# Kernel tuning notes

Hardware: AMD Instinct MI355X
Metric: run time of the kernel (lower is better)

Reference implementation:

```python
import jax, jax.numpy as jnp
import numpy as np

N = 40000
IN_DIM = 128
HID = 64
E = 640000


def sage_conv(x, edge_index, W_l, b_l, W_r):
    """PyG SAGEConv with mean aggregation.
    out = lin_l(mean_{j in N(i)} x_j) + lin_r(x_i)
    edge_index[0]=src (message source), edge_index[1]=dst (aggregation target).
    """
    src, dst = edge_index[0], edge_index[1]
    n = x.shape[0]
    msgs = x[src]                                            # [E, d] gather
    sums = jax.ops.segment_sum(msgs, dst, num_segments=n)    # [N, d]
    cnt = jax.ops.segment_sum(jnp.ones((msgs.shape[0],), x.dtype), dst,
                              num_segments=n)                # [N]
    mean = sums / jnp.maximum(cnt, 1.0)[:, None]
    return mean @ W_l.T + b_l + x @ W_r.T


def setup_inputs() -> dict:
    key = jax.random.key(0)
    ks = jax.random.split(key, 8)
    x = jax.random.normal(ks[0], (N, IN_DIM), dtype=jnp.float32)
    edge_index = jax.random.randint(ks[1], (2, E), 0, N, dtype=jnp.int32)
    s1 = 1.0 / np.sqrt(IN_DIM)
    s2 = 1.0 / np.sqrt(HID)
    W1_l = jax.random.uniform(ks[2], (HID, IN_DIM), jnp.float32, -s1, s1)
    b1_l = jax.random.uniform(ks[3], (HID,), jnp.float32, -s1, s1)
    W1_r = jax.random.uniform(ks[4], (HID, IN_DIM), jnp.float32, -s1, s1)
    W2_l = jax.random.uniform(ks[5], (HID, HID), jnp.float32, -s2, s2)
    b2_l = jax.random.uniform(ks[6], (HID,), jnp.float32, -s2, s2)
    W2_r = jax.random.uniform(ks[7], (HID, HID), jnp.float32, -s2, s2)
    return {"x": x, "edge_index": edge_index,
            "W1_l": W1_l, "b1_l": b1_l, "W1_r": W1_r,
            "W2_l": W2_l, "b2_l": b2_l, "W2_r": W2_r}


def reference(x, edge_index, W1_l, b1_l, W1_r, W2_l, b2_l, W2_r):
    h = sage_conv(x, edge_index, W1_l, b1_l, W1_r)
    h = jax.nn.relu(h)
    # dropout is identity in eval mode (reference baseline is deterministic)
    z = sage_conv(h, edge_index, W2_l, b2_l, W2_r)
    return z
```

## Files before the change

### kernel.cpp

```cpp
#include <hip/hip_runtime.h>

#define INDIM 128
#define HID 64
#define CAP 64
#define GEMM_BLOCKS 625
#define BIN_BLOCKS 256
#define PREP_BLOCKS 32
#define RSH 7
#define RMASK ((1 << RSH) - 1)
#define NRANGE 313
#define SBCAP 28

__device__ __forceinline__ float bf2f(unsigned short u) {
    union { unsigned int i; float f; } c; c.i = ((unsigned int)u) << 16; return c.f;
}
__device__ __forceinline__ unsigned short f2bf(float f) {
    union { float f; unsigned int i; } c; c.f = f;
    return (unsigned short)((c.i + 0x7FFFu + ((c.i >> 16) & 1u)) >> 16);
}

__device__ __forceinline__ void agg8(const unsigned short* __restrict__ Pb,
                                     int idx0, int deg, int q, int f8,
                                     float acc[8]) {
    const int nstep = (deg + 7) >> 3;
    for (int s = 0; s < nstep; s += 2) {
        #pragma unroll
        for (int u = 0; u < 2; ++u) {
            const int ss = s + u;
            const int lanesel = ss * 8 + q;
            const int sidx = __shfl(idx0, lanesel, 64);
            const float m = (ss < nstep && lanesel < deg) ? 1.f : 0.f;
            const uint4 v = *(const uint4*)&Pb[(size_t)sidx * 64 + f8 * 8];
            acc[0] += bf2f((unsigned short)(v.x & 0xffffu)) * m;
            acc[1] += bf2f((unsigned short)(v.x >> 16)) * m;
            acc[2] += bf2f((unsigned short)(v.y & 0xffffu)) * m;
            acc[3] += bf2f((unsigned short)(v.y >> 16)) * m;
            acc[4] += bf2f((unsigned short)(v.z & 0xffffu)) * m;
            acc[5] += bf2f((unsigned short)(v.z >> 16)) * m;
            acc[6] += bf2f((unsigned short)(v.w & 0xffffu)) * m;
            acc[7] += bf2f((unsigned short)(v.w >> 16)) * m;
        }
    }
    #pragma unroll
    for (int j = 0; j < 8; ++j) {
        acc[j] += __shfl_xor(acc[j], 8, 64);
        acc[j] += __shfl_xor(acc[j], 16, 64);
        acc[j] += __shfl_xor(acc[j], 32, 64);
    }
}


__global__ __launch_bounds__(256) void k_bin_prep(
    const int* __restrict__ src, const int* __restrict__ dst,
    unsigned int* __restrict__ hist_global, unsigned int* __restrict__ ebin,
    const float* __restrict__ W1l, const float* __restrict__ W1r,
    const float* __restrict__ W2l, const float* __restrict__ W2r,
    float* __restrict__ WT1l, float* __restrict__ WT1r,
    float* __restrict__ WT2l, float* __restrict__ WT2r, int E) {
    const int tid = threadIdx.x;

    if (blockIdx.x >= BIN_BLOCKS) {
        const int gtid = (blockIdx.x - BIN_BLOCKS) * 256 + tid;
        if (gtid < 64 * 128) {
            int j = gtid >> 7, k = gtid & 127;
            WT1l[k * 64 + j] = W1l[gtid];
            WT1r[k * 64 + j] = W1r[gtid];
        }
        if (gtid < 64 * 64) {
            int j = gtid >> 6, k = gtid & 63;
            WT2l[k * 64 + j] = W2l[gtid];
            WT2r[k * 64 + j] = W2r[gtid];
        }
        return;
    }

    __shared__ unsigned int hist[NRANGE];
    __shared__ unsigned int cur[NRANGE];
    const int b = blockIdx.x;
    const int ech = (E + BIN_BLOCKS - 1) / BIN_BLOCKS;
    const int e0 = b * ech;
    const int e1 = (e0 + ech < E) ? e0 + ech : E;

    for (int r = tid; r < NRANGE; r += 256) { hist[r] = 0; cur[r] = 0; }
    __syncthreads();
    for (int e = e0 + tid; e < e1; e += 256)
        atomicAdd(&hist[((unsigned)dst[e]) >> RSH], 1u);
    __syncthreads();
    for (int r = tid; r < NRANGE; r += 256)
        hist_global[(size_t)r * BIN_BLOCKS + b] = hist[r];
    __syncthreads();
    for (int e = e0 + tid; e < e1; e += 256) {
        const unsigned d = (unsigned)dst[e];
        const unsigned s = (unsigned)src[e];
        const unsigned r = d >> RSH;
        const unsigned off = atomicAdd(&cur[r], 1u);
        if (off < SBCAP)
            ebin[((size_t)r * BIN_BLOCKS + b) * SBCAP + off] = (d << 16) | s;
    }
}


__global__ __launch_bounds__(256) void k_gemm1_place(
    const float* __restrict__ A,
    const float* __restrict__ WTl, const float* __restrict__ WTr,
    unsigned short* __restrict__ Pb, float* __restrict__ Q,
    const unsigned int* __restrict__ hist_global,
    const unsigned int* __restrict__ ebin,
    int* __restrict__ cnt, unsigned short* __restrict__ sorted, int N) {
    __shared__ float As[64][INDIM + 1];
    __shared__ unsigned int lcnt[1 << RSH];
    const int tid = threadIdx.x;

    if (blockIdx.x < NRANGE) {
        const int r = blockIdx.x;
        if (tid < (1 << RSH)) lcnt[tid] = 0;
        __syncthreads();
        unsigned c = hist_global[(size_t)r * BIN_BLOCKS + tid];
        if (c > SBCAP) c = SBCAP;
        const unsigned int* eb = ebin + ((size_t)r * BIN_BLOCKS + tid) * SBCAP;
        for (unsigned i = 0; i < c; ++i) {
            const unsigned p = eb[i];
            const unsigned d = p >> 16;
            const unsigned slot = atomicAdd(&lcnt[d & RMASK], 1u);
            if (slot < CAP)
                sorted[(d << 6) + slot] = (unsigned short)(p & 0xffffu);
        }
        __syncthreads();
        for (int l = tid; l < (1 << RSH); l += 256) {
            const int node = (r << RSH) + l;
            if (node < N) cnt[node] = (int)lcnt[l];
        }
        return;
    }

    const int bm = (blockIdx.x - NRANGE) * 64;
    for (int idx = tid; idx < 64 * 32; idx += 256) {
        int row = idx >> 5, kq = idx & 31;
        const float4 v = ((const float4*)A)[(size_t)(bm + row) * 32 + kq];
        As[row][kq * 4 + 0] = v.x; As[row][kq * 4 + 1] = v.y;
        As[row][kq * 4 + 2] = v.z; As[row][kq * 4 + 3] = v.w;
    }
    __syncthreads();

    const int tx = tid & 15, ty = tid >> 4;
    const int n0 = ty * 4;
    float accl[4][4] = {}, accr[4][4] = {};
    #pragma unroll 8
    for (int k = 0; k < INDIM; ++k) {
        float a[4];
        #pragma unroll
        for (int i = 0; i < 4; ++i) a[i] = As[n0 + i][k];
        const float4 blv = ((const float4*)WTl)[k * 16 + tx];
        const float4 brv = ((const float4*)WTr)[k * 16 + tx];
        const float bl[4] = {blv.x, blv.y, blv.z, blv.w};
        const float br[4] = {brv.x, brv.y, brv.z, brv.w};
        #pragma unroll
        for (int i = 0; i < 4; ++i) {
            #pragma unroll
            for (int j = 0; j < 4; ++j) {
                accl[i][j] += a[i] * bl[j];
                accr[i][j] += a[i] * br[j];
            }
        }
    }
    #pragma unroll
    for (int i = 0; i < 4; ++i) {
        int m = bm + n0 + i;
        ushort4 pv;
        pv.x = f2bf(accl[i][0]); pv.y = f2bf(accl[i][1]);
        pv.z = f2bf(accl[i][2]); pv.w = f2bf(accl[i][3]);
        ((ushort4*)Pb)[(size_t)m * 16 + tx] = pv;
        ((float4*)Q)[(size_t)m * 16 + tx] =
            make_float4(accr[i][0], accr[i][1], accr[i][2], accr[i][3]);
    }
}


__global__ __launch_bounds__(256) void k_agg1(
    const unsigned short* __restrict__ Pb, const float* __restrict__ Q,
    const float* __restrict__ b1,
    const int* __restrict__ cnt, const unsigned short* __restrict__ sorted,
    unsigned short* __restrict__ Hb, float* __restrict__ H, int N) {
    const int wid  = (blockIdx.x * 256 + threadIdx.x) >> 6;
    const int lane = threadIdx.x & 63;
    const int q = lane >> 3, f8 = lane & 7;
    if (wid >= N) return;
    int deg = cnt[wid]; if (deg > CAP) deg = CAP;
    const int ls = (lane < deg) ? lane : ((deg > 0) ? deg - 1 : 0);
    const int idx0 = (deg > 0) ? (int)sorted[(wid << 6) + ls] : 0;
    float acc[8] = {};
    agg8(Pb, idx0, deg, q, f8, acc);
    if (q == 0) {
        const float inv = 1.0f / fmaxf((float)deg, 1.0f);
        const float4 qa = *(const float4*)&Q[(size_t)wid * 64 + f8 * 8];
        const float4 qb = *(const float4*)&Q[(size_t)wid * 64 + f8 * 8 + 4];
        const float4 ba = *(const float4*)&b1[f8 * 8];
        const float4 bb = *(const float4*)&b1[f8 * 8 + 4];
        float h0 = fmaxf(acc[0] * inv + ba.x + qa.x, 0.f);
        float h1 = fmaxf(acc[1] * inv + ba.y + qa.y, 0.f);
        float h2 = fmaxf(acc[2] * inv + ba.z + qa.z, 0.f);
        float h3 = fmaxf(acc[3] * inv + ba.w + qa.w, 0.f);
        float h4 = fmaxf(acc[4] * inv + bb.x + qb.x, 0.f);
        float h5 = fmaxf(acc[5] * inv + bb.y + qb.y, 0.f);
        float h6 = fmaxf(acc[6] * inv + bb.z + qb.z, 0.f);
        float h7 = fmaxf(acc[7] * inv + bb.w + qb.w, 0.f);
        uint4 u;
        u.x = (unsigned)f2bf(h0) | ((unsigned)f2bf(h1) << 16);
        u.y = (unsigned)f2bf(h2) | ((unsigned)f2bf(h3) << 16);
        u.z = (unsigned)f2bf(h4) | ((unsigned)f2bf(h5) << 16);
        u.w = (unsigned)f2bf(h6) | ((unsigned)f2bf(h7) << 16);
        *(uint4*)&Hb[(size_t)wid * 64 + f8 * 8] = u;
        *(float4*)&H[(size_t)wid * 64 + f8 * 8] = make_float4(h0, h1, h2, h3);
        *(float4*)&H[(size_t)wid * 64 + f8 * 8 + 4] = make_float4(h4, h5, h6, h7);
    }
}


__global__ __launch_bounds__(256) void k_agg2h(
    const unsigned short* __restrict__ Hb,
    const int* __restrict__ cnt, const unsigned short* __restrict__ sorted,
    float* __restrict__ meanH, int N) {
    const int wid  = (blockIdx.x * 256 + threadIdx.x) >> 6;
    const int lane = threadIdx.x & 63;
    const int q = lane >> 3, f8 = lane & 7;
    if (wid >= N) return;
    int deg = cnt[wid]; if (deg > CAP) deg = CAP;
    const int ls = (lane < deg) ? lane : ((deg > 0) ? deg - 1 : 0);
    const int idx0 = (deg > 0) ? (int)sorted[(wid << 6) + ls] : 0;
    float acc[8] = {};
    agg8(Hb, idx0, deg, q, f8, acc);
    if (q == 0) {
        const float inv = 1.0f / fmaxf((float)deg, 1.0f);
        *(float4*)&meanH[(size_t)wid * 64 + f8 * 8] =
            make_float4(acc[0] * inv, acc[1] * inv, acc[2] * inv, acc[3] * inv);
        *(float4*)&meanH[(size_t)wid * 64 + f8 * 8 + 4] =
            make_float4(acc[4] * inv, acc[5] * inv, acc[6] * inv, acc[7] * inv);
    }
}


__global__ __launch_bounds__(256) void k_gemm_z(
    const float* __restrict__ meanH, const float* __restrict__ H,
    const float* __restrict__ WTl, const float* __restrict__ WTr,
    const float* __restrict__ b2, float* __restrict__ z, int N) {
    __shared__ float As1[64][HID + 1];
    __shared__ float As2[64][HID + 1];
    const int tid = threadIdx.x;
    const int bm = blockIdx.x * 64;
    for (int idx = tid; idx < 64 * 16; idx += 256) {
        int row = idx >> 4, kq = idx & 15;
        const float4 v1 = ((const float4*)meanH)[(size_t)(bm + row) * 16 + kq];
        const float4 v2 = ((const float4*)H)[(size_t)(bm + row) * 16 + kq];
        As1[row][kq * 4 + 0] = v1.x; As1[row][kq * 4 + 1] = v1.y;
        As1[row][kq * 4 + 2] = v1.z; As1[row][kq * 4 + 3] = v1.w;
        As2[row][kq * 4 + 0] = v2.x; As2[row][kq * 4 + 1] = v2.y;
        As2[row][kq * 4 + 2] = v2.z; As2[row][kq * 4 + 3] = v2.w;
    }
    __syncthreads();

    const int tx = tid & 15, ty = tid >> 4;
    const int n0 = ty * 4;
    float acc[4][4] = {};
    #pragma unroll 8
    for (int k = 0; k < HID; ++k) {
        float a1[4], a2[4];
        #pragma unroll
        for (int i = 0; i < 4; ++i) { a1[i] = As1[n0 + i][k]; a2[i] = As2[n0 + i][k]; }
        const float4 blv = ((const float4*)WTl)[k * 16 + tx];
        const float4 brv = ((const float4*)WTr)[k * 16 + tx];
        const float bl[4] = {blv.x, blv.y, blv.z, blv.w};
        const float br[4] = {brv.x, brv.y, brv.z, brv.w};
        #pragma unroll
        for (int i = 0; i < 4; ++i) {
            #pragma unroll
            for (int j = 0; j < 4; ++j)
                acc[i][j] += a1[i] * bl[j] + a2[i] * br[j];
        }
    }
    const float4 bv = *(const float4*)&b2[tx * 4];
    #pragma unroll
    for (int i = 0; i < 4; ++i) {
        int m = bm + n0 + i;
        if (m < N) {
            ((float4*)z)[(size_t)m * 16 + tx] =
                make_float4(acc[i][0] + bv.x, acc[i][1] + bv.y,
                            acc[i][2] + bv.z, acc[i][3] + bv.w);
        }
    }
}


extern "C" void kernel_launch(void* const* d_in, const int* in_sizes, int n_in,
                              void* d_out, int out_size, void* d_ws, size_t ws_size,
                              hipStream_t stream) {
    const float* x   = (const float*)d_in[0];
    const int*  edge = (const int*)d_in[1];
    const float* W1l = (const float*)d_in[2];
    const float* b1l = (const float*)d_in[3];
    const float* W1r = (const float*)d_in[4];
    const float* W2l = (const float*)d_in[5];
    const float* b2l = (const float*)d_in[6];
    const float* W2r = (const float*)d_in[7];

    const int N = in_sizes[0] / INDIM;
    const int E = in_sizes[1] / 2;
    const int* src = edge;
    const int* dst = edge + E;

    char* w = (char*)d_ws;
    auto carve = [&](size_t bytes) {
        char* p = w; w += (bytes + 255) & ~(size_t)255; return p;
    };
    unsigned short* Pb  = (unsigned short*)carve((size_t)N * 64 * 2);
    unsigned short* Hb  = (unsigned short*)carve((size_t)N * 64 * 2);
    float* Q     = (float*)carve((size_t)N * 64 * 4);
    float* H     = (float*)carve((size_t)N * 64 * 4);
    float* meanH = (float*)carve((size_t)N * 64 * 4);
    float* WT1l = (float*)carve(128 * 64 * 4);
    float* WT1r = (float*)carve(128 * 64 * 4);
    float* WT2l = (float*)carve(64 * 64 * 4);
    float* WT2r = (float*)carve(64 * 64 * 4);
    int* cnt    = (int*)carve((size_t)N * 4);
    unsigned short* sorted = (unsigned short*)carve((size_t)N * CAP * 2);
    unsigned int* hist_global = (unsigned int*)carve((size_t)NRANGE * BIN_BLOCKS * 4);
    unsigned int* ebin = (unsigned int*)carve((size_t)NRANGE * BIN_BLOCKS * SBCAP * 4);

    float* zout = (float*)d_out;

    const int gT = (N + 63) / 64;
    const int gW = (N * 64 + 255) / 256;

    k_bin_prep<<<BIN_BLOCKS + PREP_BLOCKS, 256, 0, stream>>>(
        src, dst, hist_global, ebin,
        W1l, W1r, W2l, W2r, WT1l, WT1r, WT2l, WT2r, E);
    k_gemm1_place<<<NRANGE + GEMM_BLOCKS, 256, 0, stream>>>(
        x, WT1l, WT1r, Pb, Q, hist_global, ebin, cnt, sorted, N);
    k_agg1<<<gW, 256, 0, stream>>>(Pb, Q, b1l, cnt, sorted, Hb, H, N);
    k_agg2h<<<gW, 256, 0, stream>>>(Hb, cnt, sorted, meanH, N);
    k_gemm_z<<<gT, 256, 0, stream>>>(meanH, H, WT2l, WT2r, b2l, zout, N);
}
```

Measured before the change: 109.9 us.

## Aggregate with 32 lanes per edge row and parallelize bin placement across lanes

Measured after the change: 108.8 us. About the same (-0.9%).

```diff
diff --git a/kernel.cpp b/kernel.cpp
--- a/kernel.cpp
+++ b/kernel.cpp
@@ -11,42 +11,32 @@
 #define NRANGE 313
 #define SBCAP 28
 
-__device__ __forceinline__ float bf2f(unsigned short u) {
-    union { unsigned int i; float f; } c; c.i = ((unsigned int)u) << 16; return c.f;
-}
 __device__ __forceinline__ unsigned short f2bf(float f) {
     union { float f; unsigned int i; } c; c.f = f;
     return (unsigned short)((c.i + 0x7FFFu + ((c.i >> 16) & 1u)) >> 16);
 }
 
-__device__ __forceinline__ void agg8(const unsigned short* __restrict__ Pb,
-                                     int idx0, int deg, int q, int f8,
-                                     float acc[8]) {
-    const int nstep = (deg + 7) >> 3;
-    for (int s = 0; s < nstep; s += 2) {
-        #pragma unroll
-        for (int u = 0; u < 2; ++u) {
-            const int ss = s + u;
-            const int lanesel = ss * 8 + q;
-            const int sidx = __shfl(idx0, lanesel, 64);
-            const float m = (ss < nstep && lanesel < deg) ? 1.f : 0.f;
-            const uint4 v = *(const uint4*)&Pb[(size_t)sidx * 64 + f8 * 8];
-            acc[0] += bf2f((unsigned short)(v.x & 0xffffu)) * m;
-            acc[1] += bf2f((unsigned short)(v.x >> 16)) * m;
-            acc[2] += bf2f((unsigned short)(v.y & 0xffffu)) * m;
-            acc[3] += bf2f((unsigned short)(v.y >> 16)) * m;
-            acc[4] += bf2f((unsigned short)(v.z & 0xffffu)) * m;
-            acc[5] += bf2f((unsigned short)(v.z >> 16)) * m;
-            acc[6] += bf2f((unsigned short)(v.w & 0xffffu)) * m;
-            acc[7] += bf2f((unsigned short)(v.w >> 16)) * m;
-        }
-    }
-    #pragma unroll
-    for (int j = 0; j < 8; ++j) {
-        acc[j] += __shfl_xor(acc[j], 8, 64);
-        acc[j] += __shfl_xor(acc[j], 16, 64);
-        acc[j] += __shfl_xor(acc[j], 32, 64);
-    }
+__device__ __forceinline__ void aggF(const unsigned short* __restrict__ T,
+                                     int idxv, int deg, int f2,
+                                     float& a0, float& a1) {
+    const int eo = (threadIdx.x & 63) >> 5;
+    for (int s = 0; s < deg; s += 8) {
+        #pragma unroll
+        for (int u = 0; u < 4; ++u) {
+            const int e = s + u * 2 + eo;
+            int sidx = __shfl(idxv, e, 64);
+            const bool live = (e < deg);
+            sidx = live ? sidx : 0;
+            const unsigned uu = *(const unsigned*)&T[(size_t)sidx * 64 + f2 * 2];
+            union { unsigned i; float f; } clo, chi;
+            clo.i = uu << 16;
+            chi.i = uu & 0xffff0000u;
+            a0 += live ? clo.f : 0.f;
+            a1 += live ? chi.f : 0.f;
+        }
+    }
+    a0 += __shfl_xor(a0, 32, 64);
+    a1 += __shfl_xor(a1, 32, 64);
 }
 
 
@@ -115,15 +105,23 @@
         const int r = blockIdx.x;
         if (tid < (1 << RSH)) lcnt[tid] = 0;
         __syncthreads();
-        unsigned c = hist_global[(size_t)r * BIN_BLOCKS + tid];
-        if (c > SBCAP) c = SBCAP;
-        const unsigned int* eb = ebin + ((size_t)r * BIN_BLOCKS + tid) * SBCAP;
-        for (unsigned i = 0; i < c; ++i) {
-            const unsigned p = eb[i];
-            const unsigned d = p >> 16;
-            const unsigned slot = atomicAdd(&lcnt[d & RMASK], 1u);
-            if (slot < CAP)
-                sorted[(d << 6) + slot] = (unsigned short)(p & 0xffffu);
+        const int lane = tid & 63, w = tid >> 6;
+        const int sb_local = lane >> 3, ent0 = lane & 7;
+        for (int g = w * 8; g < BIN_BLOCKS; g += 32) {
+            const int sb = g + sb_local;
+            unsigned c = hist_global[(size_t)r * BIN_BLOCKS + sb];
+            if (c > SBCAP) c = SBCAP;
+            const unsigned int* eb = ebin + ((size_t)r * BIN_BLOCKS + sb) * SBCAP;
+            for (unsigned p = 0; p * 8 < c; ++p) {
+                const unsigned e = p * 8 + ent0;
+                if (e < c) {
+                    const unsigned pkt = eb[e];
+                    const unsigned d = pkt >> 16;
+                    const unsigned slot = atomicAdd(&lcnt[d & RMASK], 1u);
+                    if (slot < CAP)
+                        sorted[(d << 6) + slot] = (unsigned short)(pkt & 0xffffu);
+                }
+            }
         }
         __syncthreads();
         for (int l = tid; l < (1 << RSH); l += 256) {
@@ -183,35 +181,21 @@
     unsigned short* __restrict__ Hb, float* __restrict__ H, int N) {
     const int wid  = (blockIdx.x * 256 + threadIdx.x) >> 6;
     const int lane = threadIdx.x & 63;
-    const int q = lane >> 3, f8 = lane & 7;
+    const int f2 = lane & 31;
     if (wid >= N) return;
     int deg = cnt[wid]; if (deg > CAP) deg = CAP;
-    const int ls = (lane < deg) ? lane : ((deg > 0) ? deg - 1 : 0);
-    const int idx0 = (deg > 0) ? (int)sorted[(wid << 6) + ls] : 0;
-    float acc[8] = {};
-    agg8(Pb, idx0, deg, q, f8, acc);
-    if (q == 0) {
+    const int idxv = (int)sorted[(wid << 6) + lane];
+    float a0 = 0.f, a1 = 0.f;
+    aggF(Pb, idxv, deg, f2, a0, a1);
+    if (lane < 32) {
         const float inv = 1.0f / fmaxf((float)deg, 1.0f);
-        const float4 qa = *(const float4*)&Q[(size_t)wid * 64 + f8 * 8];
-        const float4 qb = *(const float4*)&Q[(size_t)wid * 64 + f8 * 8 + 4];
-        const float4 ba = *(const float4*)&b1[f8 * 8];
-        const float4 bb = *(const float4*)&b1[f8 * 8 + 4];
-        float h0 = fmaxf(acc[0] * inv + ba.x + qa.x, 0.f);
-        float h1 = fmaxf(acc[1] * inv + ba.y + qa.y, 0.f);
-        float h2 = fmaxf(acc[2] * inv + ba.z + qa.z, 0.f);
-        float h3 = fmaxf(acc[3] * inv + ba.w + qa.w, 0.f);
-        float h4 = fmaxf(acc[4] * inv + bb.x + qb.x, 0.f);
-        float h5 = fmaxf(acc[5] * inv + bb.y + qb.y, 0.f);
-        float h6 = fmaxf(acc[6] * inv + bb.z + qb.z, 0.f);
-        float h7 = fmaxf(acc[7] * inv + bb.w + qb.w, 0.f);
-        uint4 u;
-        u.x = (unsigned)f2bf(h0) | ((unsigned)f2bf(h1) << 16);
-        u.y = (unsigned)f2bf(h2) | ((unsigned)f2bf(h3) << 16);
-        u.z = (unsigned)f2bf(h4) | ((unsigned)f2bf(h5) << 16);
-        u.w = (unsigned)f2bf(h6) | ((unsigned)f2bf(h7) << 16);
-        *(uint4*)&Hb[(size_t)wid * 64 + f8 * 8] = u;
-        *(float4*)&H[(size_t)wid * 64 + f8 * 8] = make_float4(h0, h1, h2, h3);
-        *(float4*)&H[(size_t)wid * 64 + f8 * 8 + 4] = make_float4(h4, h5, h6, h7);
+        const float2 qv = *(const float2*)&Q[(size_t)wid * 64 + f2 * 2];
+        const float2 bv = *(const float2*)&b1[f2 * 2];
+        const float h0 = fmaxf(a0 * inv + bv.x + qv.x, 0.f);
+        const float h1 = fmaxf(a1 * inv + bv.y + qv.y, 0.f);
+        *(unsigned*)&Hb[(size_t)wid * 64 + f2 * 2] =
+            (unsigned)f2bf(h0) | ((unsigned)f2bf(h1) << 16);
+        *(float2*)&H[(size_t)wid * 64 + f2 * 2] = make_float2(h0, h1);
     }
 }
 
@@ -222,19 +206,16 @@
     float* __restrict__ meanH, int N) {
     const int wid  = (blockIdx.x * 256 + threadIdx.x) >> 6;
     const int lane = threadIdx.x & 63;
-    const int q = lane >> 3, f8 = lane & 7;
+    const int f2 = lane & 31;
     if (wid >= N) return;
     int deg = cnt[wid]; if (deg > CAP) deg = CAP;
-    const int ls = (lane < deg) ? lane : ((deg > 0) ? deg - 1 : 0);
-    const int idx0 = (deg > 0) ? (int)sorted[(wid << 6) + ls] : 0;
-    float acc[8] = {};
-    agg8(Hb, idx0, deg, q, f8, acc);
-    if (q == 0) {
+    const int idxv = (int)sorted[(wid << 6) + lane];
+    float a0 = 0.f, a1 = 0.f;
+    aggF(Hb, idxv, deg, f2, a0, a1);
+    if (lane < 32) {
         const float inv = 1.0f / fmaxf((float)deg, 1.0f);
-        *(float4*)&meanH[(size_t)wid * 64 + f8 * 8] =
-            make_float4(acc[0] * inv, acc[1] * inv, acc[2] * inv, acc[3] * inv);
-        *(float4*)&meanH[(size_t)wid * 64 + f8 * 8 + 4] =
-            make_float4(acc[4] * inv, acc[5] * inv, acc[6] * inv, acc[7] * inv);
+        *(float2*)&meanH[(size_t)wid * 64 + f2 * 2] =
+            make_float2(a0 * inv, a1 * inv);
     }
 }
 
```
